# Kernel optimization log

Measured on AMD Instinct MI355X. Metric: run time of the kernel, lower is better.

## Reference

```python
import jax, jax.numpy as jnp
import numpy as np

BETA = 0.25  # commitment weight from config['beta']


def _mlp(h, ws, bs):
    # MLPLayers: Linear + ReLU between hidden layers, no activation after last.
    n = len(ws)
    for i in range(n):
        h = h @ ws[i] + bs[i]
        if i < n - 1:
            h = jax.nn.relu(h)
    return h


def setup_inputs() -> dict:
    key = jax.random.key(0)
    ks = jax.random.split(key, 16)
    B, IN = 65536, 768
    dims = [768, 512, 256, 128]  # [in_dim] + layers + [e_dim]
    d = {"x": jax.random.normal(ks[0], (B, IN), dtype=jnp.float32)}
    # encoder weights
    for i in range(3):
        fan_in = dims[i]
        d[f"enc_w{i}"] = jax.random.normal(ks[1 + i], (dims[i], dims[i + 1]), dtype=jnp.float32) / np.sqrt(fan_in)
        d[f"enc_b{i}"] = jnp.zeros((dims[i + 1],), dtype=jnp.float32)
    rdims = dims[::-1]
    for i in range(3):
        d[f"dec_w{i}"] = jax.random.normal(ks[4 + i], (rdims[i], rdims[i + 1]), dtype=jnp.float32) / np.sqrt(rdims[i])
        d[f"dec_b{i}"] = jnp.zeros((rdims[i + 1],), dtype=jnp.float32)
    # 4 residual levels, 256 codes each, e_dim=128
    d["codebooks"] = jax.random.normal(ks[7], (4, 256, 128), dtype=jnp.float32)
    return d


def reference(x, enc_w0, enc_b0, enc_w1, enc_b1, enc_w2, enc_b2,
              dec_w0, dec_b0, dec_w1, dec_b1, dec_w2, dec_b2, codebooks):
    sg = jax.lax.stop_gradient
    z = _mlp(x, [enc_w0, enc_w1, enc_w2], [enc_b0, enc_b1, enc_b2])  # (B, e_dim)

    residual = z
    x_q = jnp.zeros_like(z)
    losses = []
    n_levels = codebooks.shape[0]
    for l in range(n_levels):
        C = codebooks[l]  # (K, e_dim)
        # squared L2 distances (B, K) via expansion, avoids materializing diffs
        dist = (jnp.sum(residual * residual, axis=1, keepdims=True)
                - 2.0 * residual @ C.T
                + jnp.sum(C * C, axis=1))
        idx = jnp.argmin(dist, axis=1)  # (B,)
        q = C[idx]                      # (B, e_dim) gather
        # codebook loss + beta * commitment loss
        losses.append(jnp.mean((sg(q) - residual) ** 2)
                      + BETA * jnp.mean((q - sg(residual)) ** 2))
        x_q = x_q + q
        residual = residual - sg(q)
    rq_loss = jnp.mean(jnp.stack(losses))

    # straight-through estimator
    y_q = z + sg(x_q - z)
    y = _mlp(y_q, [dec_w0, dec_w1, dec_w2], [dec_b0, dec_b1, dec_b2])  # (B, in_dim)
    return y, rq_loss
```

## Files before the change

### kernel.cpp

```cpp
#include <hip/hip_runtime.h>
#include <cstdint>
#include <cstddef>


typedef _Float16 F16;
typedef F16  v8h __attribute__((ext_vector_type(8)));
typedef float v4f __attribute__((ext_vector_type(4)));

__device__ __forceinline__ void gload_lds16(const void* g, void* l) {
    __builtin_amdgcn_global_load_lds(
        (const __attribute__((address_space(1))) void*)g,
        (__attribute__((address_space(3))) void*)l, 16, 0, 0);
}

__device__ __forceinline__ void split2(float v, F16& h, F16& l) {
    h = (F16)v;
    l = (F16)((v - (float)h) * 2048.0f);
}

template<bool RELU, bool HASBIAS>
__global__ __launch_bounds__(256, 2)
void f16gemm_kernel(const float* __restrict__ A, const F16* __restrict__ Bh,
                    const F16* __restrict__ Bl, const float* __restrict__ bias,
                    float* __restrict__ C, int M, int N, int K)
{
    __shared__ v8h As[1024];
    __shared__ v8h Bs[1024];

    const int tid  = threadIdx.x;
    const int lane = tid & 63;
    const int wid  = tid >> 6;
    const int wr   = wid >> 1;
    const int wc   = wid & 1;
    const long bm  = (long)blockIdx.x * 128;
    const long bn  = (long)blockIdx.y * 128;

    const int sm = tid & 127;
    const int sc = tid >> 7;
    const float* aSrc = A + (bm + sm) * (long)K + sc * 8;

    const int bc = (lane & 7) ^ (lane >> 3);
    const F16* bSrcBase[4];
    void* bDst[4];
    #pragma unroll
    for (int jj = 0; jj < 4; jj++) {
        int j  = wid * 4 + jj;
        long n = bn + j * 8 + (lane >> 3);
        bSrcBase[jj] = (bc < 4) ? (Bh + n * (long)K + bc * 8)
                                : (Bl + n * (long)K + (bc - 4) * 8);
        bDst[jj] = (void*)(Bs + j * 64);
    }

    const int cq = lane >> 4;
    int aOff[4], bOff[4];
    #pragma unroll
    for (int i = 0; i < 4; i++) {
        int am  = wr * 64 + i * 16 + (lane & 15);
        aOff[i] = am * 8 + (cq ^ (am & 7));
        int bn2 = wc * 64 + i * 16 + (lane & 15);
        bOff[i] = bn2 * 8 + (cq ^ (bn2 & 7));
    }

    v4f acc[4][4]  = {};
    v4f accx[4][4] = {};

    for (int k0 = 0; k0 < K; k0 += 32) {
        #pragma unroll
        for (int jj = 0; jj < 4; jj++)
            gload_lds16(bSrcBase[jj] + k0, bDst[jj]);

        #pragma unroll
        for (int i = 0; i < 2; i++) {
            const float* s = aSrc + k0 + i * 16;
            float4 v0 = *reinterpret_cast<const float4*>(s);
            float4 v1 = *reinterpret_cast<const float4*>(s + 4);
            float vv[8] = {v0.x, v0.y, v0.z, v0.w, v1.x, v1.y, v1.z, v1.w};
            v8h hi, lo;
            #pragma unroll
            for (int e = 0; e < 8; e++) { F16 h, l; split2(vv[e], h, l); hi[e] = h; lo[e] = l; }
            int ph = (sc + 2 * i) ^ (sm & 7);
            As[sm * 8 + ph]       = hi;
            As[sm * 8 + (ph ^ 4)] = lo;
        }
        __syncthreads();

        v8h bh[4], bl[4];
        #pragma unroll
        for (int ni = 0; ni < 4; ni++) {
            bh[ni] = Bs[bOff[ni]];
            bl[ni] = Bs[bOff[ni] ^ 4];
        }
        #pragma unroll
        for (int mi = 0; mi < 4; mi++) {
            v8h ah = As[aOff[mi]];
            v8h al = As[aOff[mi] ^ 4];
            #pragma unroll
            for (int ni = 0; ni < 4; ni++) {
                acc[mi][ni]  = __builtin_amdgcn_mfma_f32_16x16x32_f16(ah, bh[ni], acc[mi][ni],  0, 0, 0);
                accx[mi][ni] = __builtin_amdgcn_mfma_f32_16x16x32_f16(ah, bl[ni], accx[mi][ni], 0, 0, 0);
                accx[mi][ni] = __builtin_amdgcn_mfma_f32_16x16x32_f16(al, bh[ni], accx[mi][ni], 0, 0, 0);
            }
        }
        __syncthreads();
    }

    const int rbase = (lane >> 4) * 4;
    const int cl    = lane & 15;
    #pragma unroll
    for (int ni = 0; ni < 4; ni++) {
        long col = bn + wc * 64 + ni * 16 + cl;
        float bv = 0.0f;
        if constexpr (HASBIAS) bv = bias[col];
        #pragma unroll
        for (int mi = 0; mi < 4; mi++) {
            #pragma unroll
            for (int r = 0; r < 4; r++) {
                long row = bm + wr * 64 + mi * 16 + rbase + r;
                float v = acc[mi][ni][r] + accx[mi][ni][r] * (1.0f / 2048.0f) + bv;
                if constexpr (RELU) v = fmaxf(v, 0.0f);
                C[row * (long)N + col] = v;
            }
        }
    }
}

__global__ void wprep_kernel(const float* __restrict__ W, F16* __restrict__ H,
                             F16* __restrict__ L, int K, int N)
{
    int i = blockIdx.x * 256 + threadIdx.x;
    if (i >= K * N) return;
    int k = i / N, n = i % N;
    float v = W[i];
    F16 h, l; split2(v, h, l);
    H[(long)n * K + k] = h;
    L[(long)n * K + k] = l;
}

__global__ void cbprep_kernel(const float* __restrict__ Cb, F16* __restrict__ H,
                              F16* __restrict__ L)
{
    int i = blockIdx.x * 256 + threadIdx.x;
    float v = Cb[i];
    F16 h, l; split2(v, h, l);
    H[i] = h; L[i] = l;
}

__global__ __launch_bounds__(256)
void rq_update_kernel(const float* __restrict__ scores,
                      const float* __restrict__ cb,
                      const float* __restrict__ src,
                      float* __restrict__ resid,
                      float* __restrict__ xq,
                      float* __restrict__ lossF,
                      int M, int first)
{
    __shared__ float c2s[256];
    __shared__ float lsum[4];
    const int tid  = threadIdx.x;
    const int lane = tid & 63;
    const int wave = tid >> 6;

    {   float s = 0.f;
        #pragma unroll
        for (int d = 0; d < 128; d += 4) {
            float4 v = *reinterpret_cast<const float4*>(cb + (long)tid * 128 + d);
            s += v.x * v.x + v.y * v.y + v.z * v.z + v.w * v.w;
        }
        c2s[tid] = s;
    }
    __syncthreads();

    float myloss = 0.f;
    const int stride = gridDim.x * 4;
    for (int row = blockIdx.x * 4 + wave; row < M; row += stride) {
        const float* srow = scores + (long)row * 256;
        float best = 3.4e38f; int bidx = 0;
        #pragma unroll
        for (int j = 0; j < 4; j++) {
            int code = lane + j * 64;
            float d = fmaf(-2.f, srow[code], c2s[code]);
            if (d < best) { best = d; bidx = code; }
        }
        #pragma unroll
        for (int off = 32; off > 0; off >>= 1) {
            float ob = __shfl_down(best, off);
            int   oi = __shfl_down(bidx, off);
            if (ob < best || (ob == best && oi < bidx)) { best = ob; bidx = oi; }
        }
        bidx = __shfl(bidx, 0);

        long base = (long)row * 128 + lane * 2;
        float2 r = *reinterpret_cast<const float2*>(src + base);
        float2 q = *reinterpret_cast<const float2*>(cb + (long)bidx * 128 + lane * 2);
        float dx = r.x - q.x, dy = r.y - q.y;
        myloss += dx * dx + dy * dy;
        float2 nr; nr.x = dx; nr.y = dy;
        *reinterpret_cast<float2*>(resid + base) = nr;
        if (first) {
            float2 qv; qv.x = q.x; qv.y = q.y;
            *reinterpret_cast<float2*>(xq + base) = qv;
        } else {
            float2 xv = *reinterpret_cast<float2*>(xq + base);
            xv.x += q.x; xv.y += q.y;
            *reinterpret_cast<float2*>(xq + base) = xv;
        }
    }

    #pragma unroll
    for (int off = 32; off > 0; off >>= 1) myloss += __shfl_down(myloss, off);
    if (lane == 0) lsum[wave] = myloss;
    __syncthreads();
    if (tid == 0) atomicAdd(lossF, (lsum[0] + lsum[1]) + (lsum[2] + lsum[3]));
}

__global__ void zero4_kernel(float* __restrict__ F)
{
    if (threadIdx.x < 4) F[threadIdx.x] = 0.f;
}

__global__ void finalize_loss_kernel(const float* __restrict__ F, float* __restrict__ out)
{
    if (threadIdx.x == 0) {
        float s = (F[0] + F[1]) + (F[2] + F[3]);
        out[0] = s * (1.25f / (4.f * 65536.f * 128.f));
    }
}

extern "C" void kernel_launch(void* const* d_in, const int* in_sizes, int n_in,
                              void* d_out, int out_size, void* d_ws, size_t ws_size,
                              hipStream_t stream)
{
    const float* x      = (const float*)d_in[0];
    const float* enc_w0 = (const float*)d_in[1];
    const float* enc_b0 = (const float*)d_in[2];
    const float* enc_w1 = (const float*)d_in[3];
    const float* enc_b1 = (const float*)d_in[4];
    const float* enc_w2 = (const float*)d_in[5];
    const float* enc_b2 = (const float*)d_in[6];
    const float* dec_w0 = (const float*)d_in[7];
    const float* dec_b0 = (const float*)d_in[8];
    const float* dec_w1 = (const float*)d_in[9];
    const float* dec_b1 = (const float*)d_in[10];
    const float* dec_w2 = (const float*)d_in[11];
    const float* dec_b2 = (const float*)d_in[12];
    const float* codebooks = (const float*)d_in[13];

    const int M = 65536;
    float* ws   = (float*)d_ws;

    float* bufA   = ws;
    float* bufB   = ws + 33554432;
    float* z      = bufA;
    float* resid  = bufA + 8388608;
    float* xq     = bufA + 16777216;
    float* scores = bufB;
    float* y      = (float*)d_out;

    F16* e0h = (F16*)d_out;          F16* e0l = e0h + 393216;
    F16* e1h = e0l + 393216;         F16* e1l = e1h + 131072;
    F16* e2h = e1l + 131072;         F16* e2l = e2h + 32768;
    F16* d0h = e2l + 32768;          F16* d0l = d0h + 32768;
    F16* d1h = d0l + 32768;          F16* d1l = d1h + 131072;
    F16* cbh = d1l + 131072;         F16* cbl = cbh + 131072;
    float* F = (float*)d_out + 2000000;
    F16* d2h = (F16*)bufB;           F16* d2l = d2h + 393216;

    dim3 blk(256);

    wprep_kernel<<<dim3(1536), blk, 0, stream>>>(enc_w0, e0h, e0l, 768, 512);
    wprep_kernel<<<dim3(512),  blk, 0, stream>>>(enc_w1, e1h, e1l, 512, 256);
    wprep_kernel<<<dim3(128),  blk, 0, stream>>>(enc_w2, e2h, e2l, 256, 128);
    wprep_kernel<<<dim3(128),  blk, 0, stream>>>(dec_w0, d0h, d0l, 128, 256);
    wprep_kernel<<<dim3(512),  blk, 0, stream>>>(dec_w1, d1h, d1l, 256, 512);
    cbprep_kernel<<<dim3(512), blk, 0, stream>>>(codebooks, cbh, cbl);
    zero4_kernel<<<dim3(1), dim3(64), 0, stream>>>(F);

    f16gemm_kernel<true,  true><<<dim3(512, 4), blk, 0, stream>>>(x,    e0h, e0l, enc_b0, bufA, M, 512, 768);
    f16gemm_kernel<true,  true><<<dim3(512, 2), blk, 0, stream>>>(bufA, e1h, e1l, enc_b1, bufB, M, 256, 512);
    f16gemm_kernel<false, true><<<dim3(512, 1), blk, 0, stream>>>(bufB, e2h, e2l, enc_b2, z,    M, 128, 256);

    for (int l = 0; l < 4; l++) {
        const float* cb  = codebooks + (long)l * 32768;
        const float* src = (l == 0) ? z : resid;
        f16gemm_kernel<false, false><<<dim3(512, 2), blk, 0, stream>>>(src, cbh + l * 32768, cbl + l * 32768,
                                                                       nullptr, scores, M, 256, 128);
        rq_update_kernel<<<dim3(1024), blk, 0, stream>>>(scores, cb, src, resid, xq, F + l, M, (l == 0) ? 1 : 0);
    }
    finalize_loss_kernel<<<dim3(1), dim3(64), 0, stream>>>(F, y + 50331648);

    f16gemm_kernel<true,  true><<<dim3(512, 2), blk, 0, stream>>>(xq,   d0h, d0l, dec_b0, bufB, M, 256, 128);
    f16gemm_kernel<true,  true><<<dim3(512, 4), blk, 0, stream>>>(bufB, d1h, d1l, dec_b1, bufA, M, 512, 256);
    wprep_kernel<<<dim3(1536), blk, 0, stream>>>(dec_w2, d2h, d2l, 512, 768);
    f16gemm_kernel<false, true><<<dim3(512, 6), blk, 0, stream>>>(bufA, d2h, d2l, dec_b2, y,    M, 768, 512);
}
```

Before: 1.264 ms.

## Pre-split activations to fp16 hi/lo and double-buffer GEMM LDS loads

The GEMM now takes activations already split into fp16 hi/lo planes. These come from a new x-split kernel and from the epilogues of earlier GEMMs and the RQ update. This lets the A tile be loaded with direct global-to-LDS copies instead of per-iteration conversion in registers. The k-loop is double-buffered so the next tile loads while MFMAs run, and block indices are remapped for L2 locality. The trade-off is extra HBM traffic to write and read the split planes, larger LDS use, and a reworked workspace aliasing layout that risks buffer overlap bugs.

```diff
diff --git a/kernel.cpp b/kernel.cpp
--- a/kernel.cpp
+++ b/kernel.cpp
@@ -4,8 +4,10 @@
 
 
 typedef _Float16 F16;
-typedef F16  v8h __attribute__((ext_vector_type(8)));
-typedef float v4f __attribute__((ext_vector_type(4)));
+typedef F16   v8h  __attribute__((ext_vector_type(8)));
+typedef F16   v2h  __attribute__((ext_vector_type(2)));
+typedef F16   v4h  __attribute__((ext_vector_type(4)));
+typedef float v4f  __attribute__((ext_vector_type(4)));
 
 __device__ __forceinline__ void gload_lds16(const void* g, void* l) {
     __builtin_amdgcn_global_load_lds(
@@ -18,40 +20,44 @@
     l = (F16)((v - (float)h) * 2048.0f);
 }
 
-template<bool RELU, bool HASBIAS>
+template<bool RELU, bool HASBIAS, bool WF32, bool WSPLIT>
 __global__ __launch_bounds__(256, 2)
-void f16gemm_kernel(const float* __restrict__ A, const F16* __restrict__ Bh,
-                    const F16* __restrict__ Bl, const float* __restrict__ bias,
-                    float* __restrict__ C, int M, int N, int K)
-{
-    __shared__ v8h As[1024];
-    __shared__ v8h Bs[1024];
+void f16gemm2(const F16* __restrict__ Ah, const F16* __restrict__ Al,
+              const F16* __restrict__ Bh, const F16* __restrict__ Bl,
+              const float* __restrict__ bias,
+              float* __restrict__ C, F16* __restrict__ Ch, F16* __restrict__ Cl,
+              int N, int K, int nbn)
+{
+    __shared__ v8h As[2048];
+    __shared__ v8h Bs[2048];
 
     const int tid  = threadIdx.x;
     const int lane = tid & 63;
     const int wid  = tid >> 6;
-    const int wr   = wid >> 1;
-    const int wc   = wid & 1;
-    const long bm  = (long)blockIdx.x * 128;
-    const long bn  = (long)blockIdx.y * 128;
-
-    const int sm = tid & 127;
-    const int sc = tid >> 7;
-    const float* aSrc = A + (bm + sm) * (long)K + sc * 8;
-
-    const int bc = (lane & 7) ^ (lane >> 3);
-    const F16* bSrcBase[4];
-    void* bDst[4];
+
+    const int nb  = gridDim.x;
+    const int cpx = nb >> 3;
+    const int sw  = (blockIdx.x & 7) * cpx + (blockIdx.x >> 3);
+    const int mt  = sw / nbn;
+    const int nt_ = sw - mt * nbn;
+    const long bm = (long)mt * 128;
+    const long bn = (long)nt_ * 128;
+
+    const int rr = lane >> 3;
+    const int c  = (lane & 7) ^ rr;
+    const F16* aS[4]; const F16* bS[4];
+    int dOf[4];
     #pragma unroll
     for (int jj = 0; jj < 4; jj++) {
-        int j  = wid * 4 + jj;
-        long n = bn + j * 8 + (lane >> 3);
-        bSrcBase[jj] = (bc < 4) ? (Bh + n * (long)K + bc * 8)
-                                : (Bl + n * (long)K + (bc - 4) * 8);
-        bDst[jj] = (void*)(Bs + j * 64);
+        int rloc = wid * 32 + jj * 8;
+        long ag = bm + rloc + rr, bg = bn + rloc + rr;
+        aS[jj] = (c < 4) ? (Ah + ag * (long)K + c * 8) : (Al + ag * (long)K + (c - 4) * 8);
+        bS[jj] = (c < 4) ? (Bh + bg * (long)K + c * 8) : (Bl + bg * (long)K + (c - 4) * 8);
+        dOf[jj] = rloc * 8;
     }
 
     const int cq = lane >> 4;
+    const int wr = wid >> 1, wc = wid & 1;
     int aOff[4], bOff[4];
     #pragma unroll
     for (int i = 0; i < 4; i++) {
@@ -64,43 +70,39 @@
     v4f acc[4][4]  = {};
     v4f accx[4][4] = {};
 
-    for (int k0 = 0; k0 < K; k0 += 32) {
-        #pragma unroll
-        for (int jj = 0; jj < 4; jj++)
-            gload_lds16(bSrcBase[jj] + k0, bDst[jj]);
-
-        #pragma unroll
-        for (int i = 0; i < 2; i++) {
-            const float* s = aSrc + k0 + i * 16;
-            float4 v0 = *reinterpret_cast<const float4*>(s);
-            float4 v1 = *reinterpret_cast<const float4*>(s + 4);
-            float vv[8] = {v0.x, v0.y, v0.z, v0.w, v1.x, v1.y, v1.z, v1.w};
-            v8h hi, lo;
-            #pragma unroll
-            for (int e = 0; e < 8; e++) { F16 h, l; split2(vv[e], h, l); hi[e] = h; lo[e] = l; }
-            int ph = (sc + 2 * i) ^ (sm & 7);
-            As[sm * 8 + ph]       = hi;
-            As[sm * 8 + (ph ^ 4)] = lo;
-        }
-        __syncthreads();
-
-        v8h bh[4], bl[4];
-        #pragma unroll
-        for (int ni = 0; ni < 4; ni++) {
-            bh[ni] = Bs[bOff[ni]];
-            bl[ni] = Bs[bOff[ni] ^ 4];
-        }
-        #pragma unroll
-        for (int mi = 0; mi < 4; mi++) {
-            v8h ah = As[aOff[mi]];
-            v8h al = As[aOff[mi] ^ 4];
+    auto stage = [&](int buf, int k0) {
+        v8h* Ab = As + buf * 1024;
+        v8h* Bb = Bs + buf * 1024;
+        #pragma unroll
+        for (int jj = 0; jj < 4; jj++) gload_lds16(aS[jj] + k0, Ab + dOf[jj]);
+        #pragma unroll
+        for (int jj = 0; jj < 4; jj++) gload_lds16(bS[jj] + k0, Bb + dOf[jj]);
+    };
+
+    const int nsteps = K >> 5;
+    stage(0, 0);
+    __syncthreads();
+
+    for (int t = 0; t < nsteps; ++t) {
+        const int cur = t & 1;
+        if (t + 1 < nsteps) stage(cur ^ 1, (t + 1) * 32);
+
+        const v8h* Ab = As + cur * 1024;
+        const v8h* Bb = Bs + cur * 1024;
+        v8h ah[4], al[4], bh[4], bl[4];
+        #pragma unroll
+        for (int i = 0; i < 4; i++) {
+            ah[i] = Ab[aOff[i]]; al[i] = Ab[aOff[i] ^ 4];
+            bh[i] = Bb[bOff[i]]; bl[i] = Bb[bOff[i] ^ 4];
+        }
+        #pragma unroll
+        for (int mi = 0; mi < 4; mi++)
             #pragma unroll
             for (int ni = 0; ni < 4; ni++) {
-                acc[mi][ni]  = __builtin_amdgcn_mfma_f32_16x16x32_f16(ah, bh[ni], acc[mi][ni],  0, 0, 0);
-                accx[mi][ni] = __builtin_amdgcn_mfma_f32_16x16x32_f16(ah, bl[ni], accx[mi][ni], 0, 0, 0);
-                accx[mi][ni] = __builtin_amdgcn_mfma_f32_16x16x32_f16(al, bh[ni], accx[mi][ni], 0, 0, 0);
+                acc[mi][ni]  = __builtin_amdgcn_mfma_f32_16x16x32_f16(ah[mi], bh[ni], acc[mi][ni],  0, 0, 0);
+                accx[mi][ni] = __builtin_amdgcn_mfma_f32_16x16x32_f16(ah[mi], bl[ni], accx[mi][ni], 0, 0, 0);
+                accx[mi][ni] = __builtin_amdgcn_mfma_f32_16x16x32_f16(al[mi], bh[ni], accx[mi][ni], 0, 0, 0);
             }
-        }
         __syncthreads();
     }
 
@@ -118,7 +120,12 @@
                 long row = bm + wr * 64 + mi * 16 + rbase + r;
                 float v = acc[mi][ni][r] + accx[mi][ni][r] * (1.0f / 2048.0f) + bv;
                 if constexpr (RELU) v = fmaxf(v, 0.0f);
-                C[row * (long)N + col] = v;
+                if constexpr (WF32) C[row * (long)N + col] = v;
+                if constexpr (WSPLIT) {
+                    F16 h, l; split2(v, h, l);
+                    Ch[row * (long)N + col] = h;
+                    Cl[row * (long)N + col] = l;
+                }
             }
         }
     }
@@ -145,14 +152,32 @@
     H[i] = h; L[i] = l;
 }
 
+__global__ void xsplit_kernel(const float* __restrict__ X, F16* __restrict__ H,
+                              F16* __restrict__ L, long n4)
+{
+    long stride = (long)gridDim.x * 256;
+    for (long i = blockIdx.x * 256 + threadIdx.x; i < n4; i += stride) {
+        float4 v = reinterpret_cast<const float4*>(X)[i];
+        v4h h, l; F16 hh, ll;
+        split2(v.x, hh, ll); h[0] = hh; l[0] = ll;
+        split2(v.y, hh, ll); h[1] = hh; l[1] = ll;
+        split2(v.z, hh, ll); h[2] = hh; l[2] = ll;
+        split2(v.w, hh, ll); h[3] = hh; l[3] = ll;
+        reinterpret_cast<v4h*>(H)[i] = h;
+        reinterpret_cast<v4h*>(L)[i] = l;
+    }
+}
+
 __global__ __launch_bounds__(256)
 void rq_update_kernel(const float* __restrict__ scores,
                       const float* __restrict__ cb,
                       const float* __restrict__ src,
                       float* __restrict__ resid,
+                      F16* __restrict__ residh, F16* __restrict__ residl,
                       float* __restrict__ xq,
+                      F16* __restrict__ xqh, F16* __restrict__ xql,
                       float* __restrict__ lossF,
-                      int M, int first)
+                      int M, int first, int last)
 {
     __shared__ float c2s[256];
     __shared__ float lsum[4];
@@ -194,15 +219,30 @@
         float2 q = *reinterpret_cast<const float2*>(cb + (long)bidx * 128 + lane * 2);
         float dx = r.x - q.x, dy = r.y - q.y;
         myloss += dx * dx + dy * dy;
-        float2 nr; nr.x = dx; nr.y = dy;
-        *reinterpret_cast<float2*>(resid + base) = nr;
-        if (first) {
-            float2 qv; qv.x = q.x; qv.y = q.y;
-            *reinterpret_cast<float2*>(xq + base) = qv;
+
+        if (!last) {
+            float2 nr; nr.x = dx; nr.y = dy;
+            *reinterpret_cast<float2*>(resid + base) = nr;
+            v2h nh, nl; F16 h, l;
+            split2(dx, h, l); nh[0] = h; nl[0] = l;
+            split2(dy, h, l); nh[1] = h; nl[1] = l;
+            *reinterpret_cast<v2h*>(residh + base) = nh;
+            *reinterpret_cast<v2h*>(residl + base) = nl;
+        }
+        float2 xv;
+        if (first) { xv.x = q.x; xv.y = q.y; }
+        else {
+            xv = *reinterpret_cast<float2*>(xq + base);
+            xv.x += q.x; xv.y += q.y;
+        }
+        if (!last) {
+            *reinterpret_cast<float2*>(xq + base) = xv;
         } else {
-            float2 xv = *reinterpret_cast<float2*>(xq + base);
-            xv.x += q.x; xv.y += q.y;
-            *reinterpret_cast<float2*>(xq + base) = xv;
+            v2h nh, nl; F16 h, l;
+            split2(xv.x, h, l); nh[0] = h; nl[0] = l;
+            split2(xv.y, h, l); nh[1] = h; nl[1] = l;
+            *reinterpret_cast<v2h*>(xqh + base) = nh;
+            *reinterpret_cast<v2h*>(xql + base) = nl;
         }
     }
 
@@ -246,24 +286,39 @@
     const float* codebooks = (const float*)d_in[13];
 
     const int M = 65536;
-    float* ws   = (float*)d_ws;
-
-    float* bufA   = ws;
-    float* bufB   = ws + 33554432;
-    float* z      = bufA;
-    float* resid  = bufA + 8388608;
-    float* xq     = bufA + 16777216;
-    float* scores = bufB;
-    float* y      = (float*)d_out;
-
-    F16* e0h = (F16*)d_out;          F16* e0l = e0h + 393216;
-    F16* e1h = e0l + 393216;         F16* e1l = e1h + 131072;
-    F16* e2h = e1l + 131072;         F16* e2l = e2h + 32768;
-    F16* d0h = e2l + 32768;          F16* d0l = d0h + 32768;
-    F16* d1h = d0l + 32768;          F16* d1l = d1h + 131072;
-    F16* cbh = d1l + 131072;         F16* cbl = cbh + 131072;
-    float* F = (float*)d_out + 2000000;
-    F16* d2h = (F16*)bufB;           F16* d2l = d2h + 393216;
+
+    F16*   wsF = (F16*)d_ws;
+    float* wsf = (float*)d_ws;
+    F16*   Xh  = wsF;
+    F16*   Xl  = wsF + 50331648;
+    float* z   = wsf;
+    F16*   zh  = wsF + 16777216;
+    F16*   zl  = wsF + 25165824;
+    F16*   g2l = wsF;
+    F16*   g2h = wsF + 33554432;
+    F16*   h2h = wsF + 67108864;
+    F16*   h2l = wsF + 83886080;
+    float* scores = wsf + 33554432;
+    F16*   g1h = wsF + 67108864;
+    F16*   g1l = wsF + 83886080;
+    F16*   d2h = wsF + 67108864;
+    F16*   d2l = d2h + 393216;
+
+    F16*   doF = (F16*)d_out;
+    float* y   = (float*)d_out;
+    F16*   h1h = doF;
+    F16*   h1l = doF + 33554432;
+    float* xq  = (float*)d_out;
+    F16*   xqh = doF + 16777216;
+    F16*   xql = doF + 25165824;
+    F16*   w_  = doF + 67108864;
+    F16* e0h = w_;              F16* e0l = e0h + 393216;
+    F16* e1h = e0l + 393216;    F16* e1l = e1h + 131072;
+    F16* e2h = e1l + 131072;    F16* e2l = e2h + 32768;
+    F16* d0h = e2l + 32768;     F16* d0l = d0h + 32768;
+    F16* d1h = d0l + 32768;     F16* d1l = d1h + 131072;
+    F16* cbh = d1l + 131072;    F16* cbl = cbh + 131072;
+    float* F = (float*)d_out + 35000000;
 
     dim3 blk(256);
 
@@ -273,23 +328,25 @@
     wprep_kernel<<<dim3(128),  blk, 0, stream>>>(dec_w0, d0h, d0l, 128, 256);
     wprep_kernel<<<dim3(512),  blk, 0, stream>>>(dec_w1, d1h, d1l, 256, 512);
     cbprep_kernel<<<dim3(512), blk, 0, stream>>>(codebooks, cbh, cbl);
+    xsplit_kernel<<<dim3(4096), blk, 0, stream>>>(x, Xh, Xl, 12582912);
     zero4_kernel<<<dim3(1), dim3(64), 0, stream>>>(F);
 
-    f16gemm_kernel<true,  true><<<dim3(512, 4), blk, 0, stream>>>(x,    e0h, e0l, enc_b0, bufA, M, 512, 768);
-    f16gemm_kernel<true,  true><<<dim3(512, 2), blk, 0, stream>>>(bufA, e1h, e1l, enc_b1, bufB, M, 256, 512);
-    f16gemm_kernel<false, true><<<dim3(512, 1), blk, 0, stream>>>(bufB, e2h, e2l, enc_b2, z,    M, 128, 256);
+    f16gemm2<true,  true, false, true ><<<dim3(2048), blk, 0, stream>>>(Xh, Xl, e0h, e0l, enc_b0, nullptr, h1h, h1l, 512, 768, 4);
+    f16gemm2<true,  true, false, true ><<<dim3(1024), blk, 0, stream>>>(h1h, h1l, e1h, e1l, enc_b1, nullptr, h2h, h2l, 256, 512, 2);
+    f16gemm2<false, true, true,  true ><<<dim3(512),  blk, 0, stream>>>(h2h, h2l, e2h, e2l, enc_b2, z, zh, zl, 128, 256, 1);
 
     for (int l = 0; l < 4; l++) {
-        const float* cb  = codebooks + (long)l * 32768;
-        const float* src = (l == 0) ? z : resid;
-        f16gemm_kernel<false, false><<<dim3(512, 2), blk, 0, stream>>>(src, cbh + l * 32768, cbl + l * 32768,
-                                                                       nullptr, scores, M, 256, 128);
-        rq_update_kernel<<<dim3(1024), blk, 0, stream>>>(scores, cb, src, resid, xq, F + l, M, (l == 0) ? 1 : 0);
+        const float* cb = codebooks + (long)l * 32768;
+        const float* src = (l == 0) ? z : z;
+        f16gemm2<false, false, true, false><<<dim3(1024), blk, 0, stream>>>(zh, zl, cbh + l * 32768, cbl + l * 32768,
+                                                                            nullptr, scores, nullptr, nullptr, 256, 128, 2);
+        rq_update_kernel<<<dim3(1024), blk, 0, stream>>>(scores, cb, src, z, zh, zl, xq, xqh, xql,
+                                                         F + l, M, (l == 0) ? 1 : 0, (l == 3) ? 1 : 0);
     }
     finalize_loss_kernel<<<dim3(1), dim3(64), 0, stream>>>(F, y + 50331648);
 
-    f16gemm_kernel<true,  true><<<dim3(512, 2), blk, 0, stream>>>(xq,   d0h, d0l, dec_b0, bufB, M, 256, 128);
-    f16gemm_kernel<true,  true><<<dim3(512, 4), blk, 0, stream>>>(bufB, d1h, d1l, dec_b1, bufA, M, 512, 256);
+    f16gemm2<true,  true, false, true ><<<dim3(1024), blk, 0, stream>>>(xqh, xql, d0h, d0l, dec_b0, nullptr, g1h, g1l, 256, 128, 2);
+    f16gemm2<true,  true, false, true ><<<dim3(2048), blk, 0, stream>>>(g1h, g1l, d1h, d1l, dec_b1, nullptr, g2h, g2l, 512, 256, 4);
     wprep_kernel<<<dim3(1536), blk, 0, stream>>>(dec_w2, d2h, d2l, 512, 768);
-    f16gemm_kernel<false, true><<<dim3(512, 6), blk, 0, stream>>>(bufA, d2h, d2l, dec_b2, y,    M, 768, 512);
-}
+    f16gemm2<false, true, true,  false><<<dim3(3072), blk, 0, stream>>>(g2h, g2l, d2h, d2l, dec_b2, y, nullptr, nullptr, 768, 512, 6);
+}
```

New measurement: 1.311 ms. 1.04x slower.
